# Kernel optimization log

Hardware: AMD Instinct MI355X
Metric: run time of the kernel (lower is better)

Reference implementation:

```python
import jax, jax.numpy as jnp
import numpy as np
from jax import lax

B = 8192
HS = 64        # hidden_size (output channels)
HS4 = HS + 4   # internal channel count (68)
K = 3          # conv kernel size


def setup_inputs() -> dict:
    key = jax.random.key(0)
    ks = jax.random.split(key, 16)
    def n(k, shape, s=1.0):
        return jax.random.normal(k, shape, dtype=jnp.float32) * s
    return {
        "x": n(ks[0], (B, HS, 6, 6)),
        "cell": n(ks[1], (B, 2)),
        "interspace_coord": n(ks[2], (B, 2, 6, 6)),
        "conv1_w": n(ks[3], (HS4, HS4, K, K), 0.05),
        "conv1_b": n(ks[4], (HS4,), 0.05),
        "conv3_w": n(ks[5], (HS4, HS4, K, K), 0.05),
        "conv3_b": n(ks[6], (HS4,), 0.05),
        "lin5_w": n(ks[7], (9 * HS, HS4 * 25), 0.02),
        "lin5_b": n(ks[8], (9 * HS,), 0.02),
        "lin4_w": n(ks[9], (9 * HS, HS4 * 16), 0.02),
        "lin4_b": n(ks[10], (9 * HS,), 0.02),
        "lin3_w": n(ks[11], (9 * HS, HS4 * 9), 0.02),
        "lin3_b": n(ks[12], (9 * HS,), 0.02),
        "final_w": n(ks[13], (HS, 9 * HS), 0.02),
        "final_b": n(ks[14], (HS,), 0.02),
    }


def _conv(z, w, b):
    # torch Conv2d with padding=k//2, stride 1 == SAME conv, NCHW/OIHW
    y = lax.conv_general_dilated(z, w, (1, 1), 'SAME',
                                 dimension_numbers=('NCHW', 'OIHW', 'NCHW'))
    return y + b[None, :, None, None]


def _corners(z, ws):
    # four corner windows, stacked on a new leading axis (corner-major)
    H, W = z.shape[-2:]
    return jnp.stack([z[..., :ws, :ws],
                      z[..., :ws, W - ws:],
                      z[..., H - ws:, :ws],
                      z[..., H - ws:, W - ws:]], axis=0)


def reference(x, cell, interspace_coord,
              conv1_w, conv1_b, conv3_w, conv3_b,
              lin5_w, lin5_b, lin4_w, lin4_b, lin3_w, lin3_b,
              final_w, final_b):
    Bn = x.shape[0]
    new_cell = jnp.broadcast_to(cell.reshape(Bn, -1)[:, :, None, None],
                                (Bn, 2, 6, 6))
    lins = {5: (lin5_w, lin5_b), 4: (lin4_w, lin4_b), 3: (lin3_w, lin3_b)}
    for ws in (5, 4, 3):
        z = jnp.concatenate([x, new_cell, interspace_coord], axis=1)  # [B,68,6,6]
        z = _corners(z, ws).reshape(-1, HS4, ws, ws)                  # [4B,68,ws,ws]
        z = jnp.sin(z) + jnp.cos(z)
        z = jax.nn.relu(_conv(z, conv1_w, conv1_b))
        z = jnp.sin(z) + jnp.cos(z)
        z = jax.nn.relu(_conv(z, conv3_w, conv3_b)).reshape(4, Bn, -1)
        Wl, bl = lins[ws]
        z = jax.nn.relu(z @ Wl.T + bl).reshape(4, Bn, HS, 3, 3)
        m = jnp.concatenate([z[0], z[1]], axis=-1)   # [B,64,3,6]
        n = jnp.concatenate([z[2], z[3]], axis=-1)
        x = jnp.concatenate([m, n], axis=-2)          # [B,64,6,6]
    ew = 3
    c = _corners(x, ew)                               # [4,B,64,3,3]
    c = c.reshape(4 * Bn, -1) @ final_w.T + final_b   # [4B,64]
    c = c.reshape(Bn, HS, 2, 2)                       # same flat-order reshape as torch
    xc = x[:, :, ew - 1:ew + 1, ew - 1:ew + 1]        # center 2x2
    return (xc * c).reshape(Bn, HS, -1)
```

## Files before the change

### kernel.cpp

```cpp
#include <hip/hip_runtime.h>
#include <hip/hip_bf16.h>
#include <cstdint>
#include <cstddef>

#define BN 8192
#define MTOT 32768

using bf16 = __hip_bfloat16;
typedef float f32x4 __attribute__((ext_vector_type(4)));
typedef short short8 __attribute__((ext_vector_type(8)));

__device__ __forceinline__ bf16 f2b(float v) { return __float2bfloat16(v); }
__device__ __forceinline__ float b2f(bf16 v) { return __bfloat162float(v); }
__device__ __forceinline__ float sincos_sum(float x) {
    return 1.41421356237f * __sinf(x + 0.78539816340f);
}


__global__ __launch_bounds__(256)
void zprep_block(const float* __restrict__ xF, const float* __restrict__ cell,
                 const float* __restrict__ isc, bf16* __restrict__ Z,
                 int m0g, int CM)
{
    constexpr int KD = 1728, KTRUE = 1700;
    const int b = blockIdx.x, tid = threadIdx.x;
    __shared__ float s[68][37];

    for (int i = tid; i < 64 * 36; i += 256) {
        int ic = i / 36, off = i % 36;
        s[ic][off] = sincos_sum(xF[((size_t)b * 64 + ic) * 36 + off]);
    }
    if (tid < 2) {
        float t = sincos_sum(cell[b * 2 + tid]);
        #pragma unroll
        for (int off = 0; off < 36; off++) s[64 + tid][off] = t;
    }
    if (tid >= 64 && tid < 136) {
        int j = tid - 64;
        int ic = j / 36, off = j % 36;
        s[66 + ic][off] = sincos_sum(isc[((size_t)b * 2 + ic) * 36 + off]);
    }
    __syncthreads();

    for (int i = tid; i < 4 * KD; i += 256) {
        int q = i / KD, k = i % KD;
        int gm = q * BN + b;
        if (gm < m0g || gm >= m0g + CM) continue;
        float v = 0.f;
        if (k < KTRUE) {
            int pi = k / 68, ic = k % 68;
            int r = (q >> 1) + pi / 5;
            int c = (q & 1) + pi % 5;
            v = s[ic][r * 6 + c];
        }
        Z[(size_t)(gm - m0g) * KD + k] = f2b(v);
    }
}

template<int WSv>
__device__ __forceinline__ bf16 conv_elem(const float* __restrict__ src, int n, int k)
{
    constexpr int KTRUE = 68 * WSv * WSv;
    float v = 0.f;
    if (n < KTRUE && k < KTRUE) {
        int po = n / 68, oc = n % 68, ro = po / WSv, co = po % WSv;
        int pi = k / 68, ic = k % 68, ri = pi / WSv, ci = pi % WSv;
        int kr = ri - ro + 1, kc = ci - co + 1;
        if (kr >= 0 && kr < 3 && kc >= 0 && kc < 3)
            v = src[((oc * 68 + ic) * 3 + kr) * 3 + kc];
    }
    return f2b(v);
}
template<int WSv>
__device__ __forceinline__ bf16 lin_elem(const float* __restrict__ wl, int n, int k)
{
    constexpr int KTRUE = 68 * WSv * WSv;
    float v = 0.f;
    if (n < 576 && k < KTRUE) {
        int pi = k / 68, ic = k % 68;
        v = wl[(size_t)n * KTRUE + ic * (WSv * WSv) + pi];
    }
    return f2b(v);
}

__global__ void megabuild(const float* __restrict__ c1w, const float* __restrict__ c3w,
                          const float* __restrict__ l5w, const float* __restrict__ l4w,
                          const float* __restrict__ l3w, const float* __restrict__ fw,
                          const float* __restrict__ c1b, const float* __restrict__ c3b,
                          const float* __restrict__ bl5, const float* __restrict__ bl4,
                          const float* __restrict__ bl3, const float* __restrict__ bfin,
                          const float* __restrict__ cell, const float* __restrict__ isc,
                          bf16* __restrict__ w1d5, bf16* __restrict__ w3d5,
                          bf16* __restrict__ w1d4, bf16* __restrict__ w3d4,
                          bf16* __restrict__ w1d3, bf16* __restrict__ w3d3,
                          bf16* __restrict__ wl5p, bf16* __restrict__ wl4p,
                          bf16* __restrict__ wl3p, bf16* __restrict__ wfp,
                          float* __restrict__ bias,
                          bf16* __restrict__ Z4, bf16* __restrict__ Z3)
{
    constexpr unsigned S0 = 2u*1792*1728, S1 = 2u*1152*1088, S2 = 2u*640*640;
    constexpr unsigned S3 = 640u*1728, S4 = 640u*1088, S5 = 640u*640;
    constexpr unsigned S6 = 128u*576, S7 = 9216;
    constexpr unsigned S8 = 4u*8192*16*4, S9 = 4u*8192*9*4, S10 = 32768u*28;
    constexpr unsigned O1=S0, O2=O1+S1, O3=O2+S2, O4=O3+S3, O5=O4+S4, O6=O5+S5,
                       O7=O6+S6, O8=O7+S7, O9=O8+S8, O10=O9+S9, OT=O10+S10;
    unsigned e = blockIdx.x * 256u + threadIdx.x;
    if (e >= OT) return;
    if (e < O1) {
        constexpr unsigned per = 1792u*1728;
        unsigned i = (e < per) ? e : e - per;
        bf16* dst = (e < per) ? w1d5 : w3d5;
        const float* src = (e < per) ? c1w : c3w;
        dst[i] = conv_elem<5>(src, (int)(i / 1728u), (int)(i % 1728u));
    } else if (e < O2) {
        unsigned i0 = e - O1; constexpr unsigned per = 1152u*1088;
        unsigned i = (i0 < per) ? i0 : i0 - per;
        bf16* dst = (i0 < per) ? w1d4 : w3d4;
        const float* src = (i0 < per) ? c1w : c3w;
        dst[i] = conv_elem<4>(src, (int)(i / 1088u), (int)(i % 1088u));
    } else if (e < O3) {
        unsigned i0 = e - O2; constexpr unsigned per = 640u*640;
        unsigned i = (i0 < per) ? i0 : i0 - per;
        bf16* dst = (i0 < per) ? w1d3 : w3d3;
        const float* src = (i0 < per) ? c1w : c3w;
        dst[i] = conv_elem<3>(src, (int)(i / 640u), (int)(i % 640u));
    } else if (e < O4) {
        unsigned i = e - O3;
        wl5p[i] = lin_elem<5>(l5w, (int)(i / 1728u), (int)(i % 1728u));
    } else if (e < O5) {
        unsigned i = e - O4;
        wl4p[i] = lin_elem<4>(l4w, (int)(i / 1088u), (int)(i % 1088u));
    } else if (e < O6) {
        unsigned i = e - O5;
        wl3p[i] = lin_elem<3>(l3w, (int)(i / 640u), (int)(i % 640u));
    } else if (e < O7) {
        unsigned i = e - O6, n = i / 576u, k = i % 576u;
        wfp[i] = (n < 64u) ? f2b(fw[n * 576u + k]) : f2b(0.f);
    } else if (e < O8) {
        int i = (int)(e - O7);
        float v = 0.f;
        if (i < 1792)      { int n = i;        if (n < 1700) v = c1b[n % 68]; }
        else if (i < 3584) { int n = i - 1792; if (n < 1700) v = c3b[n % 68]; }
        else if (i < 4736) { int n = i - 3584; if (n < 1088) v = c1b[n % 68]; }
        else if (i < 5888) { int n = i - 4736; if (n < 1088) v = c3b[n % 68]; }
        else if (i < 6528) { int n = i - 5888; if (n < 612)  v = c1b[n % 68]; }
        else if (i < 7168) { int n = i - 6528; if (n < 612)  v = c3b[n % 68]; }
        else if (i < 7808) { int n = i - 7168; if (n < 576)  v = bl5[n]; }
        else if (i < 8448) { int n = i - 7808; if (n < 576)  v = bl4[n]; }
        else if (i < 9088) { int n = i - 8448; if (n < 576)  v = bl3[n]; }
        else               { int n = i - 9088; if (n < 64)   v = bfin[n]; }
        bias[i] = v;
    } else if (e < O9) {
        unsigned i = e - O8;
        int j = (int)(i & 3u); i >>= 2;
        int pi = (int)(i & 15u); i >>= 4;
        int b = (int)(i & 8191u); int q = (int)(i >> 13);
        float t;
        if (j < 2) t = cell[b * 2 + j];
        else {
            int r = (q >> 1) * 2 + pi / 4, c = (q & 1) * 2 + pi % 4;
            t = isc[((size_t)b * 2 + (j - 2)) * 36 + r * 6 + c];
        }
        Z4[((size_t)q * BN + b) * 1088 + pi * 68 + 64 + j] = f2b(sincos_sum(t));
    } else if (e < O10) {
        unsigned i = e - O9;
        int j = (int)(i & 3u); i >>= 2;
        int pi = (int)(i % 9u); i /= 9u;
        int b = (int)(i & 8191u); int q = (int)(i >> 13);
        float t;
        if (j < 2) t = cell[b * 2 + j];
        else {
            int r = (q >> 1) * 3 + pi / 3, c = (q & 1) * 3 + pi % 3;
            t = isc[((size_t)b * 2 + (j - 2)) * 36 + r * 6 + c];
        }
        Z3[((size_t)q * BN + b) * 640 + pi * 68 + 64 + j] = f2b(sincos_sum(t));
    } else {
        unsigned i = e - O10;
        int m = (int)(i / 28u), t = (int)(i % 28u);
        Z3[(size_t)m * 640 + 612 + t] = f2b(0.f);
    }
}

__device__ __forceinline__ void gload_lds16(const bf16* g, const bf16* lds_wave_base)
{
    unsigned off = (unsigned)(uintptr_t)lds_wave_base;
    off = __builtin_amdgcn_readfirstlane(off);
    __builtin_amdgcn_global_load_lds((const __attribute__((address_space(1))) unsigned int*)g,
                                     (__attribute__((address_space(3))) unsigned int*)off,
                                     16, 0, 0);
}

__device__ __forceinline__ int imin(int a, int b) { return a < b ? a : b; }
__device__ __forceinline__ int imax(int a, int b) { return a > b ? a : b; }

template<int EPI, int WS, int WN>
__global__ __launch_bounds__(512, 4)
void gemm8(const bf16* __restrict__ A, const bf16* __restrict__ Bm, int KD,
           const float* __restrict__ bias, int ntiles,
           bf16* __restrict__ C, int ldc, int nlimit,
           int m0g, bf16* __restrict__ znext)
{
    __shared__ bf16 As[3][8192];
    __shared__ bf16 Bs[3][4096];
    const int tid = threadIdx.x;
    const int wave = tid >> 6, lane = tid & 63;
    const int l15 = lane & 15, lq = lane >> 4;
    const int wr = (wave >> 1) * 64, wc = (wave & 1) * 64;

    const int id = blockIdx.x;
    const int mt8 = (int)gridDim.x / (ntiles * 8);
    const int xcd = id & 7, local = id >> 3;
    const int m_idx = xcd * mt8 + local / ntiles;
    const int n_idx = local % ntiles;
    const int n0 = n_idx * 128, m0 = m_idx * 256;

    int s0b = 0, s0e = KD, s1b = 0, s1e = 0, s2b = 0, s2e = 0;
    if (WS > 0) {
        int po_lo = imin(n0 / 68, WS * WS - 1);
        int po_hi = imin((n0 + 127) / 68, WS * WS - 1);
        int ro_lo = po_lo / WS, ro_hi = po_hi / WS;
        int r_lo = imax(ro_lo - 1, 0), r_hi = imin(ro_hi + 1, WS - 1);
        int ci_lo = 0, ci_hi = WS - 1;
        if (ro_lo == ro_hi) {
            ci_lo = imax(po_lo % WS - 1, 0);
            ci_hi = imin(po_hi % WS + 1, WS - 1);
        }
        if (ci_lo == 0 && ci_hi == WS - 1) {
            s0b = (r_lo * WS * 68) & ~31;
            s0e = imin(KD, ((r_hi + 1) * WS * 68 + 31) & ~31);
        } else {
            s0b = ((r_lo * WS + ci_lo) * 68) & ~31;
            s0e = imin(KD, (((r_lo * WS + ci_hi + 1) * 68) + 31) & ~31);
            if (r_hi > r_lo) {
                s1b = (((r_lo + 1) * WS + ci_lo) * 68) & ~31;
                s1e = imin(KD, ((((r_lo + 1) * WS + ci_hi + 1) * 68) + 31) & ~31);
            }
            if (r_hi > r_lo + 1) {
                s2b = (((r_lo + 2) * WS + ci_lo) * 68) & ~31;
                s2e = imin(KD, ((((r_lo + 2) * WS + ci_hi + 1) * 68) + 31) & ~31);
            }
        }
    }
    const int c0 = (s0e - s0b) >> 5;
    const int c1 = c0 + ((s1e - s1b) >> 5);
    const int nt = c1 + ((s2e - s2b) >> 5);
    auto k0_of = [&](int t2) -> int {
        int k = s0b + (t2 << 5);
        if (t2 >= c0) k = s1b + ((t2 - c0) << 5);
        if (t2 >= c1) k = s2b + ((t2 - c1) << 5);
        return k;
    };

    const int srow = tid >> 2;
    const int sc8 = (tid & 3) ^ ((srow >> 1) & 3);
    const bf16* aSrc = A + (size_t)(m0 + srow) * KD + sc8 * 8;
    const bf16* bSrc = Bm + (size_t)(n0 + srow) * KD + sc8 * 8;
    const int sOff = srow * 32 + (tid & 3) * 8;

    auto stageA = [&](int k0, int buf) {
        gload_lds16(aSrc + k0, &As[buf][sOff]);
        gload_lds16(aSrc + k0 + (size_t)128 * KD, &As[buf][sOff + 4096]);
    };
    auto stageB = [&](int k0, int buf) {
        gload_lds16(bSrc + k0, &Bs[buf][sOff]);
    };

    const int swz = (lq ^ ((l15 >> 1) & 3)) * 8;
    const int offA0 = (wr + l15) * 32 + swz;
    const int offB0 = (wc + l15) * 32 + swz;

    f32x4 acc[4][4];
    #pragma unroll
    for (int i = 0; i < 4; i++)
        #pragma unroll
        for (int j = 0; j < 4; j++) { f32x4 z = {0.f, 0.f, 0.f, 0.f}; acc[i][j] = z; }

    {
        const int k0a = k0_of(0);
        stageA(k0a, 0); stageB(k0a, 0);
        if (nt > 1) {
            const int k0b = k0_of(1);
            stageA(k0b, 1); stageB(k0b, 1);
        }
        __syncthreads();
    }

    for (int t = 0; t < nt; ++t) {
        const int cur = t % 3;
        const int nx = (t + 2) % 3;
        const bool pf = (t + 2) < nt;

        const bf16* Ac = &As[cur][0];
        const bf16* Bc = &Bs[cur][0];

        short8 af[4], bg[4];
        #pragma unroll
        for (int i = 0; i < 4; i++) af[i] = *(const short8*)&Ac[offA0 + i * 512];
        #pragma unroll
        for (int j = 0; j < 4; j++) bg[j] = *(const short8*)&Bc[offB0 + j * 512];

        if (pf) {
            const int k2 = k0_of(t + 2);
            stageA(k2, nx); stageB(k2, nx);
        }

        __builtin_amdgcn_s_setprio(1);
        #pragma unroll
        for (int i = 0; i < 4; i++)
            #pragma unroll
            for (int j = 0; j < 4; j++)
                acc[i][j] = __builtin_amdgcn_mfma_f32_16x16x32_bf16(af[i], bg[j], acc[i][j], 0, 0, 0);
        __builtin_amdgcn_s_setprio(0);

        if (pf) asm volatile("s_waitcnt vmcnt(3)" ::: "memory");
        else    asm volatile("s_waitcnt vmcnt(0)" ::: "memory");
        __builtin_amdgcn_s_barrier();
    }

    float bj[4];
    #pragma unroll
    for (int j = 0; j < 4; j++) bj[j] = bias[n0 + wc + j * 16 + l15];

    #pragma unroll
    for (int i = 0; i < 4; i++) {
        #pragma unroll
        for (int j = 0; j < 4; j++) {
            int n = n0 + wc + j * 16 + l15;
            #pragma unroll
            for (int r = 0; r < 4; r++) {
                int m = m0 + wr + i * 16 + lq * 4 + r;
                float v = acc[i][j][r];
                if (EPI == 0) {
                    if (n < nlimit) {
                        v += bj[j]; v = fmaxf(v, 0.f); v = sincos_sum(v);
                        C[(size_t)m * ldc + n] = f2b(v);
                    }
                } else if (EPI == 1) {
                    if (n < nlimit) {
                        v += bj[j]; v = fmaxf(v, 0.f);
                        C[(size_t)m * ldc + n] = f2b(v);
                    }
                } else {
                    if (n < 576) {
                        v += bj[j]; v = fmaxf(v, 0.f);
                        bf16 tv = f2b(sincos_sum(v));
                        int gm = m0g + m;
                        int q = gm >> 13, b = gm & (BN - 1);
                        int ch = n / 9, p = n % 9;
                        int R = p / 3 + (q >> 1) * 3, Cc = p % 3 + (q & 1) * 3;
                        constexpr int OFF = 6 - WN;
                        constexpr int KDN = (WN == 4) ? 1088 : 640;
                        #pragma unroll
                        for (int qr = 0; qr < 2; qr++) {
                            int rr = R - OFF * qr;
                            if (rr < 0 || rr >= WN) continue;
                            #pragma unroll
                            for (int qc = 0; qc < 2; qc++) {
                                int cc = Cc - OFF * qc;
                                if (cc < 0 || cc >= WN) continue;
                                int pi = rr * WN + cc;
                                znext[((size_t)((qr * 2 + qc) * BN + b)) * KDN + pi * 68 + ch] = tv;
                            }
                        }
                    }
                }
            }
        }
    }
}

template<int EPI, int WS, int WN>
__global__ __launch_bounds__(256)
void gemm_bt(const bf16* __restrict__ A, const bf16* __restrict__ Bm, int KD,
             const float* __restrict__ bias, int ntiles,
             bf16* __restrict__ C, int ldc, int nlimit,
             int m0g, bf16* __restrict__ znext,
             const bf16* __restrict__ afin_xc, float* __restrict__ outp)
{
    __shared__ bf16 As[128 * 32];
    __shared__ bf16 Bs[128 * 32];
    const int tid = threadIdx.x;
    const int wave = tid >> 6, lane = tid & 63;
    const int l15 = lane & 15, lq = lane >> 4;
    const int wr = (wave >> 1) * 64, wc = (wave & 1) * 64;

    const int id = blockIdx.x;
    const int mt8 = (int)gridDim.x / (ntiles * 8);
    const int xcd = id & 7, local = id >> 3;
    const int m_idx = xcd * mt8 + local / ntiles;
    const int n_idx = local % ntiles;
    const int n0 = n_idx * 128, m0 = m_idx * 128;

    int nspans = 1, sbeg[4], send[4];
    sbeg[0] = 0; send[0] = KD;
    if (WS > 0) {
        int po_lo = imin(n0 / 68, WS * WS - 1);
        int po_hi = imin((n0 + 127) / 68, WS * WS - 1);
        int ro_lo = po_lo / WS, ro_hi = po_hi / WS;
        int r_lo = imax(ro_lo - 1, 0), r_hi = imin(ro_hi + 1, WS - 1);
        int ci_lo = 0, ci_hi = WS - 1;
        if (ro_lo == ro_hi) {
            ci_lo = imax(po_lo % WS - 1, 0);
            ci_hi = imin(po_hi % WS + 1, WS - 1);
        }
        if (ci_lo == 0 && ci_hi == WS - 1) {
            sbeg[0] = (r_lo * WS * 68) & ~31;
            send[0] = imin(KD, ((r_hi + 1) * WS * 68 + 31) & ~31);
        } else {
            nspans = 0;
            for (int ri = r_lo; ri <= r_hi; ri++) {
                sbeg[nspans] = ((ri * WS + ci_lo) * 68) & ~31;
                send[nspans] = imin(KD, (((ri * WS + ci_hi + 1) * 68) + 31) & ~31);
                nspans++;
            }
        }
    }

    float bj[4];
    #pragma unroll
    for (int j = 0; j < 4; j++) bj[j] = bias[n0 + wc + j * 16 + l15];

    const bf16* Ab = A + (size_t)m0 * KD;
    const bf16* Bb = Bm + (size_t)n0 * KD;
    const int srow = tid >> 2, scol = (tid & 3) * 8;
    const bf16* aG0 = Ab + (size_t)srow * KD + scol;
    const bf16* aG1 = Ab + (size_t)(srow + 64) * KD + scol;
    const bf16* bG0 = Bb + (size_t)srow * KD + scol;
    const bf16* bG1 = Bb + (size_t)(srow + 64) * KD + scol;
    const bf16* lA0 = &As[wave * 512];
    const bf16* lA1 = &As[2048 + wave * 512];
    const bf16* lB0 = &Bs[wave * 512];
    const bf16* lB1 = &Bs[2048 + wave * 512];

    f32x4 acc[4][4];
    #pragma unroll
    for (int i = 0; i < 4; i++)
        #pragma unroll
        for (int j = 0; j < 4; j++) { f32x4 z = {0.f, 0.f, 0.f, 0.f}; acc[i][j] = z; }

    for (int s = 0; s < nspans; s++) {
        for (int k0 = sbeg[s]; k0 < send[s]; k0 += 32) {
            gload_lds16(aG0 + k0, lA0);
            gload_lds16(aG1 + k0, lA1);
            gload_lds16(bG0 + k0, lB0);
            gload_lds16(bG1 + k0, lB1);
            __syncthreads();
            short8 af[4], bg[4];
            #pragma unroll
            for (int i = 0; i < 4; i++) af[i] = *(const short8*)&As[(wr + i * 16 + l15) * 32 + lq * 8];
            #pragma unroll
            for (int j = 0; j < 4; j++) bg[j] = *(const short8*)&Bs[(wc + j * 16 + l15) * 32 + lq * 8];
            #pragma unroll
            for (int i = 0; i < 4; i++)
                #pragma unroll
                for (int j = 0; j < 4; j++)
                    acc[i][j] = __builtin_amdgcn_mfma_f32_16x16x32_bf16(af[i], bg[j], acc[i][j], 0, 0, 0);
            __syncthreads();
        }
    }

    #pragma unroll
    for (int i = 0; i < 4; i++) {
        #pragma unroll
        for (int j = 0; j < 4; j++) {
            int n = n0 + wc + j * 16 + l15;
            #pragma unroll
            for (int r = 0; r < 4; r++) {
                int m = m0 + wr + i * 16 + lq * 4 + r;
                float v = acc[i][j][r];
                if (EPI == 0) {
                    if (n < nlimit) {
                        v += bj[j]; v = fmaxf(v, 0.f); v = sincos_sum(v);
                        C[(size_t)m * ldc + n] = f2b(v);
                    }
                } else if (EPI == 1) {
                    if (n < nlimit) {
                        v += bj[j]; v = fmaxf(v, 0.f);
                        C[(size_t)m * ldc + n] = f2b(v);
                    }
                } else if (EPI == 2) {
                    if (n < 576) {
                        v += bj[j]; v = fmaxf(v, 0.f);
                        bf16 t = f2b(sincos_sum(v));
                        int gm = m0g + m;
                        int q = gm >> 13, b = gm & (BN - 1);
                        int ch = n / 9, p = n % 9;
                        int R = p / 3 + (q >> 1) * 3, Cc = p % 3 + (q & 1) * 3;
                        constexpr int OFF = 6 - WN;
                        constexpr int KDN = (WN == 4) ? 1088 : 640;
                        #pragma unroll
                        for (int qr = 0; qr < 2; qr++) {
                            int rr = R - OFF * qr;
                            if (rr < 0 || rr >= WN) continue;
                            #pragma unroll
                            for (int qc = 0; qc < 2; qc++) {
                                int cc = Cc - OFF * qc;
                                if (cc < 0 || cc >= WN) continue;
                                int pi = rr * WN + cc;
                                znext[((size_t)((qr * 2 + qc) * BN + b)) * KDN + pi * 68 + ch] = t;
                            }
                        }
                    }
                } else {
                    if (n < 64) {
                        v += bj[j];
                        int gm = m0g + m;
                        int f = gm * 64 + n;
                        int b2 = f >> 8, rem = f & 255;
                        int ch2 = rem >> 2, ii = (rem >> 1) & 1, jj = rem & 1;
                        int qq = ii * 2 + jj;
                        const int offt[4] = {8, 6, 2, 0};
                        float xc = b2f(afin_xc[((size_t)qq * BN + b2) * 576 + ch2 * 9 + offt[qq]]);
                        outp[f] = v * xc;
                    }
                }
            }
        }
    }
}

extern "C" void kernel_launch(void* const* d_in, const int* in_sizes, int n_in,
                              void* d_out, int out_size, void* d_ws, size_t ws_size,
                              hipStream_t stream)
{
    const float* x    = (const float*)d_in[0];
    const float* cell = (const float*)d_in[1];
    const float* isc  = (const float*)d_in[2];
    const float* c1w  = (const float*)d_in[3];
    const float* c1b  = (const float*)d_in[4];
    const float* c3w  = (const float*)d_in[5];
    const float* c3b  = (const float*)d_in[6];
    const float* l5w  = (const float*)d_in[7];
    const float* l5b  = (const float*)d_in[8];
    const float* l4w  = (const float*)d_in[9];
    const float* l4b  = (const float*)d_in[10];
    const float* l3w  = (const float*)d_in[11];
    const float* l3b  = (const float*)d_in[12];
    const float* fw   = (const float*)d_in[13];
    const float* fb   = (const float*)d_in[14];

    char* base = (char*)d_ws;
    size_t cur = 0;
    auto take = [&](size_t bytes) -> char* {
        char* r = base + cur; cur += (bytes + 255) & ~(size_t)255; return r;
    };

    const size_t Z4B = (size_t)MTOT * 1088 * 2;
    const size_t Z3B = (size_t)MTOT * 640 * 2;
    const size_t AFB = (size_t)MTOT * 576 * 2;
    size_t wbytes = 2 * (1792ull * 1728 + 1152ull * 1088 + 640ull * 640) * 2
                  + (640ull * 1728 + 640ull * 1088 + 640ull * 640) * 2
                  + 128ull * 576 * 2 + 9216ull * 4 + 64 * 256;
    auto need = [&](int nc) -> size_t {
        return Z4B + Z3B + AFB + wbytes + 2 * ((size_t)(MTOT / nc) * 1728 * 2);
    };
    int nchunk = (ws_size >= need(1)) ? 1 : (ws_size >= need(2)) ? 2
               : (ws_size >= need(4)) ? 4 : (ws_size >= need(8)) ? 8 : 16;

    bf16* Z4   = (bf16*)take(Z4B);
    bf16* Z3   = (bf16*)take(Z3B);
    bf16* afinb = (bf16*)take(AFB);
    bf16* w1d5 = (bf16*)take(1792ull * 1728 * 2);
    bf16* w3d5 = (bf16*)take(1792ull * 1728 * 2);
    bf16* w1d4 = (bf16*)take(1152ull * 1088 * 2);
    bf16* w3d4 = (bf16*)take(1152ull * 1088 * 2);
    bf16* w1d3 = (bf16*)take(640ull * 640 * 2);
    bf16* w3d3 = (bf16*)take(640ull * 640 * 2);
    bf16* wl5p = (bf16*)take(640ull * 1728 * 2);
    bf16* wl4p = (bf16*)take(640ull * 1088 * 2);
    bf16* wl3p = (bf16*)take(640ull * 640 * 2);
    bf16* wfp  = (bf16*)take(128ull * 576 * 2);
    float* biasb = (float*)take(9216ull * 4);
    int CM = MTOT / nchunk;
    int mt = CM / 128;
    int mt2 = CM / 256;
    bf16* Za = (bf16*)take((size_t)CM * 1728 * 2);
    bf16* Zb = (bf16*)take((size_t)CM * 1728 * 2);

    {
        constexpr unsigned OT = 2u*1792*1728 + 2u*1152*1088 + 2u*640*640
                              + 640u*1728 + 640u*1088 + 640u*640 + 128u*576 + 9216
                              + 4u*8192*16*4 + 4u*8192*9*4 + 32768u*28;
        megabuild<<<(OT + 255) / 256, 256, 0, stream>>>(
            c1w, c3w, l5w, l4w, l3w, fw, c1b, c3b, l5b, l4b, l3b, fb, cell, isc,
            w1d5, w3d5, w1d4, w3d4, w1d3, w3d3, wl5p, wl4p, wl3p, wfp, biasb, Z4, Z3);
    }

    for (int c = 0; c < nchunk; c++) {
        int m0g = c * CM;
        zprep_block<<<BN, 256, 0, stream>>>(x, cell, isc, Za, m0g, CM);
        gemm8<0, 5, 0><<<14 * mt2, 512, 0, stream>>>(Za, w1d5, 1728, biasb + 0, 14,
                                                     Zb, 1728, 1728, 0, nullptr);
        gemm8<1, 5, 0><<<14 * mt2, 512, 0, stream>>>(Zb, w3d5, 1728, biasb + 1792, 14,
                                                     Za, 1728, 1728, 0, nullptr);
        gemm8<2, 0, 4><<<5 * mt2, 512, 0, stream>>>(Za, wl5p, 1728, biasb + 7168, 5,
                                                    nullptr, 0, 0, m0g, Z4);
    }
    for (int c = 0; c < nchunk; c++) {
        int m0g = c * CM;
        gemm8<0, 4, 0><<<9 * mt2, 512, 0, stream>>>(Z4 + (size_t)m0g * 1088, w1d4, 1088,
                                                    biasb + 3584, 9, Zb, 1088, 1088,
                                                    0, nullptr);
        gemm8<1, 4, 0><<<9 * mt2, 512, 0, stream>>>(Zb, w3d4, 1088, biasb + 4736, 9,
                                                    Za, 1088, 1088, 0, nullptr);
        gemm8<2, 0, 3><<<5 * mt2, 512, 0, stream>>>(Za, wl4p, 1088, biasb + 7808, 5,
                                                    nullptr, 0, 0, m0g, Z3);
    }
    for (int c = 0; c < nchunk; c++) {
        int m0g = c * CM;
        gemm8<0, 3, 0><<<5 * mt2, 512, 0, stream>>>(Z3 + (size_t)m0g * 640, w1d3, 640,
                                                    biasb + 5888, 5, Zb, 640, 640,
                                                    0, nullptr);
        gemm8<1, 3, 0><<<5 * mt2, 512, 0, stream>>>(Zb, w3d3, 640, biasb + 6528, 5,
                                                    Za, 640, 640, 0, nullptr);
        gemm8<1, 0, 0><<<5 * mt2, 512, 0, stream>>>(Za, wl3p, 640, biasb + 8448, 5,
                                                    afinb + (size_t)m0g * 576, 576, 576,
                                                    0, nullptr);
    }
    for (int c = 0; c < nchunk; c++) {
        int m0g = c * CM;
        gemm_bt<3, 0, 0><<<mt, 256, 0, stream>>>(afinb + (size_t)m0g * 576, wfp, 576,
                                                 biasb + 9088, 1, nullptr, 0, 0, m0g,
                                                 nullptr, afinb, (float*)d_out);
    }
}
```

Before: 1.228 ms.

## Make gemm8 persistent with wide-tile variant and vectorize zprep stores

The GEMM kernel becomes persistent: a fixed grid of 512 blocks loops over tiles, with an XCD-aware mapping of m tiles. A WIDE template variant uses 128x256 tiles for the ws=5 convolution GEMMs, so fewer n-tiles are needed and A rows are reused across a wider N. zprep now packs eight bf16 values into one 16-byte store instead of writing scalars. The persistent loop reduces launch and tail overhead but can unbalance load when the tile count does not divide evenly, and the wide tiles change how much of the banded K range each tile skips.

```diff
diff --git a/kernel.cpp b/kernel.cpp
--- a/kernel.cpp
+++ b/kernel.cpp
@@ -42,18 +42,26 @@
     }
     __syncthreads();
 
-    for (int i = tid; i < 4 * KD; i += 256) {
-        int q = i / KD, k = i % KD;
+    for (int i = tid; i < 4 * (KD / 8); i += 256) {
+        int q = i / (KD / 8), j8 = i % (KD / 8);
         int gm = q * BN + b;
         if (gm < m0g || gm >= m0g + CM) continue;
-        float v = 0.f;
-        if (k < KTRUE) {
-            int pi = k / 68, ic = k % 68;
-            int r = (q >> 1) + pi / 5;
-            int c = (q & 1) + pi % 5;
-            v = s[ic][r * 6 + c];
-        }
-        Z[(size_t)(gm - m0g) * KD + k] = f2b(v);
+        int kbase = j8 * 8;
+        short8 pack;
+        #pragma unroll
+        for (int u = 0; u < 8; u++) {
+            int k = kbase + u;
+            float v = 0.f;
+            if (k < KTRUE) {
+                int pi = k / 68, ic = k % 68;
+                int r = (q >> 1) + pi / 5;
+                int c = (q & 1) + pi % 5;
+                v = s[ic][r * 6 + c];
+            }
+            bf16 bv = f2b(v);
+            pack[u] = *reinterpret_cast<short*>(&bv);
+        }
+        *reinterpret_cast<short8*>(&Z[(size_t)(gm - m0g) * KD + kbase]) = pack;
     }
 }
 
@@ -193,173 +201,177 @@
 __device__ __forceinline__ int imin(int a, int b) { return a < b ? a : b; }
 __device__ __forceinline__ int imax(int a, int b) { return a > b ? a : b; }
 
-template<int EPI, int WS, int WN>
+template<int EPI, int WS, int WN, int WIDE>
 __global__ __launch_bounds__(512, 4)
 void gemm8(const bf16* __restrict__ A, const bf16* __restrict__ Bm, int KD,
-           const float* __restrict__ bias, int ntiles,
+           const float* __restrict__ bias, int ntiles, int mtiles,
            bf16* __restrict__ C, int ldc, int nlimit,
            int m0g, bf16* __restrict__ znext)
 {
-    __shared__ bf16 As[3][8192];
-    __shared__ bf16 Bs[3][4096];
+    constexpr int BMc = WIDE ? 128 : 256;
+    constexpr int BNc = WIDE ? 256 : 128;
+    constexpr int NWN = WIDE ? 4 : 2;
+    __shared__ bf16 As[3][BMc * 32];
+    __shared__ bf16 Bs[3][BNc * 32];
     const int tid = threadIdx.x;
     const int wave = tid >> 6, lane = tid & 63;
     const int l15 = lane & 15, lq = lane >> 4;
-    const int wr = (wave >> 1) * 64, wc = (wave & 1) * 64;
-
-    const int id = blockIdx.x;
-    const int mt8 = (int)gridDim.x / (ntiles * 8);
-    const int xcd = id & 7, local = id >> 3;
-    const int m_idx = xcd * mt8 + local / ntiles;
-    const int n_idx = local % ntiles;
-    const int n0 = n_idx * 128, m0 = m_idx * 256;
-
-    int s0b = 0, s0e = KD, s1b = 0, s1e = 0, s2b = 0, s2e = 0;
-    if (WS > 0) {
-        int po_lo = imin(n0 / 68, WS * WS - 1);
-        int po_hi = imin((n0 + 127) / 68, WS * WS - 1);
-        int ro_lo = po_lo / WS, ro_hi = po_hi / WS;
-        int r_lo = imax(ro_lo - 1, 0), r_hi = imin(ro_hi + 1, WS - 1);
-        int ci_lo = 0, ci_hi = WS - 1;
-        if (ro_lo == ro_hi) {
-            ci_lo = imax(po_lo % WS - 1, 0);
-            ci_hi = imin(po_hi % WS + 1, WS - 1);
-        }
-        if (ci_lo == 0 && ci_hi == WS - 1) {
-            s0b = (r_lo * WS * 68) & ~31;
-            s0e = imin(KD, ((r_hi + 1) * WS * 68 + 31) & ~31);
-        } else {
-            s0b = ((r_lo * WS + ci_lo) * 68) & ~31;
-            s0e = imin(KD, (((r_lo * WS + ci_hi + 1) * 68) + 31) & ~31);
-            if (r_hi > r_lo) {
-                s1b = (((r_lo + 1) * WS + ci_lo) * 68) & ~31;
-                s1e = imin(KD, ((((r_lo + 1) * WS + ci_hi + 1) * 68) + 31) & ~31);
-            }
-            if (r_hi > r_lo + 1) {
-                s2b = (((r_lo + 2) * WS + ci_lo) * 68) & ~31;
-                s2e = imin(KD, ((((r_lo + 2) * WS + ci_hi + 1) * 68) + 31) & ~31);
-            }
-        }
-    }
-    const int c0 = (s0e - s0b) >> 5;
-    const int c1 = c0 + ((s1e - s1b) >> 5);
-    const int nt = c1 + ((s2e - s2b) >> 5);
-    auto k0_of = [&](int t2) -> int {
-        int k = s0b + (t2 << 5);
-        if (t2 >= c0) k = s1b + ((t2 - c0) << 5);
-        if (t2 >= c1) k = s2b + ((t2 - c1) << 5);
-        return k;
-    };
+    const int wr = (wave / NWN) * 64, wc = (wave % NWN) * 64;
+
+    const int xcd = blockIdx.x & 7, lblk = blockIdx.x >> 3;
+    const int bpx = (int)gridDim.x >> 3;
+    const int mloc = mtiles >> 3;
+    const int tot = mloc * ntiles;
 
     const int srow = tid >> 2;
-    const int sc8 = (tid & 3) ^ ((srow >> 1) & 3);
-    const bf16* aSrc = A + (size_t)(m0 + srow) * KD + sc8 * 8;
-    const bf16* bSrc = Bm + (size_t)(n0 + srow) * KD + sc8 * 8;
+    const int scx = (tid & 3) ^ ((srow >> 1) & 3);
     const int sOff = srow * 32 + (tid & 3) * 8;
-
-    auto stageA = [&](int k0, int buf) {
-        gload_lds16(aSrc + k0, &As[buf][sOff]);
-        gload_lds16(aSrc + k0 + (size_t)128 * KD, &As[buf][sOff + 4096]);
-    };
-    auto stageB = [&](int k0, int buf) {
-        gload_lds16(bSrc + k0, &Bs[buf][sOff]);
-    };
-
     const int swz = (lq ^ ((l15 >> 1) & 3)) * 8;
     const int offA0 = (wr + l15) * 32 + swz;
     const int offB0 = (wc + l15) * 32 + swz;
 
-    f32x4 acc[4][4];
-    #pragma unroll
-    for (int i = 0; i < 4; i++)
-        #pragma unroll
-        for (int j = 0; j < 4; j++) { f32x4 z = {0.f, 0.f, 0.f, 0.f}; acc[i][j] = z; }
-
-    {
-        const int k0a = k0_of(0);
-        stageA(k0a, 0); stageB(k0a, 0);
-        if (nt > 1) {
-            const int k0b = k0_of(1);
-            stageA(k0b, 1); stageB(k0b, 1);
-        }
-        __syncthreads();
-    }
-
-    for (int t = 0; t < nt; ++t) {
-        const int cur = t % 3;
-        const int nx = (t + 2) % 3;
-        const bool pf = (t + 2) < nt;
-
-        const bf16* Ac = &As[cur][0];
-        const bf16* Bc = &Bs[cur][0];
-
-        short8 af[4], bg[4];
-        #pragma unroll
-        for (int i = 0; i < 4; i++) af[i] = *(const short8*)&Ac[offA0 + i * 512];
-        #pragma unroll
-        for (int j = 0; j < 4; j++) bg[j] = *(const short8*)&Bc[offB0 + j * 512];
-
-        if (pf) {
-            const int k2 = k0_of(t + 2);
-            stageA(k2, nx); stageB(k2, nx);
-        }
-
-        __builtin_amdgcn_s_setprio(1);
+    for (int w = lblk; w < tot; w += bpx) {
+        const int m_idx = (w / ntiles) * 8 + xcd;
+        const int n_idx = w % ntiles;
+        const int n0 = n_idx * BNc, m0 = m_idx * BMc;
+
+        int s0b = 0, s0e = KD, s1b = 0, s1e = 0, s2b = 0, s2e = 0;
+        if (WS > 0) {
+            int po_lo = imin(n0 / 68, WS * WS - 1);
+            int po_hi = imin((n0 + BNc - 1) / 68, WS * WS - 1);
+            int ro_lo = po_lo / WS, ro_hi = po_hi / WS;
+            int r_lo = imax(ro_lo - 1, 0), r_hi = imin(ro_hi + 1, WS - 1);
+            int ci_lo = 0, ci_hi = WS - 1;
+            if (ro_lo == ro_hi) {
+                ci_lo = imax(po_lo % WS - 1, 0);
+                ci_hi = imin(po_hi % WS + 1, WS - 1);
+            }
+            if (ci_lo == 0 && ci_hi == WS - 1) {
+                s0b = (r_lo * WS * 68) & ~31;
+                s0e = imin(KD, ((r_hi + 1) * WS * 68 + 31) & ~31);
+            } else {
+                s0b = ((r_lo * WS + ci_lo) * 68) & ~31;
+                s0e = imin(KD, (((r_lo * WS + ci_hi + 1) * 68) + 31) & ~31);
+                if (r_hi > r_lo) {
+                    s1b = (((r_lo + 1) * WS + ci_lo) * 68) & ~31;
+                    s1e = imin(KD, ((((r_lo + 1) * WS + ci_hi + 1) * 68) + 31) & ~31);
+                }
+                if (r_hi > r_lo + 1) {
+                    s2b = (((r_lo + 2) * WS + ci_lo) * 68) & ~31;
+                    s2e = imin(KD, ((((r_lo + 2) * WS + ci_hi + 1) * 68) + 31) & ~31);
+                }
+            }
+        }
+        const int c0 = (s0e - s0b) >> 5;
+        const int c1 = c0 + ((s1e - s1b) >> 5);
+        const int nt = c1 + ((s2e - s2b) >> 5);
+        auto k0_of = [&](int t2) -> int {
+            int k = s0b + (t2 << 5);
+            if (t2 >= c0) k = s1b + ((t2 - c0) << 5);
+            if (t2 >= c1) k = s2b + ((t2 - c1) << 5);
+            return k;
+        };
+
+        const bf16* aSrc = A + (size_t)(m0 + srow) * KD + scx * 8;
+        const bf16* bSrc = Bm + (size_t)(n0 + srow) * KD + scx * 8;
+
+        auto stageAll = [&](int k0, int buf) {
+            if (WIDE) {
+                gload_lds16(aSrc + k0, &As[buf][sOff]);
+                gload_lds16(bSrc + k0, &Bs[buf][sOff]);
+                gload_lds16(bSrc + k0 + (size_t)128 * KD, &Bs[buf][sOff + 4096]);
+            } else {
+                gload_lds16(aSrc + k0, &As[buf][sOff]);
+                gload_lds16(aSrc + k0 + (size_t)128 * KD, &As[buf][sOff + 4096]);
+                gload_lds16(bSrc + k0, &Bs[buf][sOff]);
+            }
+        };
+
+        f32x4 acc[4][4];
         #pragma unroll
         for (int i = 0; i < 4; i++)
             #pragma unroll
-            for (int j = 0; j < 4; j++)
-                acc[i][j] = __builtin_amdgcn_mfma_f32_16x16x32_bf16(af[i], bg[j], acc[i][j], 0, 0, 0);
-        __builtin_amdgcn_s_setprio(0);
-
-        if (pf) asm volatile("s_waitcnt vmcnt(3)" ::: "memory");
-        else    asm volatile("s_waitcnt vmcnt(0)" ::: "memory");
-        __builtin_amdgcn_s_barrier();
-    }
-
-    float bj[4];
-    #pragma unroll
-    for (int j = 0; j < 4; j++) bj[j] = bias[n0 + wc + j * 16 + l15];
-
-    #pragma unroll
-    for (int i = 0; i < 4; i++) {
+            for (int j = 0; j < 4; j++) { f32x4 z = {0.f, 0.f, 0.f, 0.f}; acc[i][j] = z; }
+
+        {
+            stageAll(k0_of(0), 0);
+            if (nt > 1) stageAll(k0_of(1), 1);
+            __syncthreads();
+        }
+
+        for (int t = 0; t < nt; ++t) {
+            const int cur = t % 3;
+            const int nx = (t + 2) % 3;
+            const bool pf = (t + 2) < nt;
+
+            const bf16* Ac = &As[cur][0];
+            const bf16* Bc = &Bs[cur][0];
+
+            short8 af[4], bg[4];
+            #pragma unroll
+            for (int i = 0; i < 4; i++) af[i] = *(const short8*)&Ac[offA0 + i * 512];
+            #pragma unroll
+            for (int j = 0; j < 4; j++) bg[j] = *(const short8*)&Bc[offB0 + j * 512];
+
+            if (pf) stageAll(k0_of(t + 2), nx);
+
+            __builtin_amdgcn_s_setprio(1);
+            #pragma unroll
+            for (int i = 0; i < 4; i++)
+                #pragma unroll
+                for (int j = 0; j < 4; j++)
+                    acc[i][j] = __builtin_amdgcn_mfma_f32_16x16x32_bf16(af[i], bg[j], acc[i][j], 0, 0, 0);
+            __builtin_amdgcn_s_setprio(0);
+
+            if (pf) asm volatile("s_waitcnt vmcnt(3)" ::: "memory");
+            else    asm volatile("s_waitcnt vmcnt(0)" ::: "memory");
+            __builtin_amdgcn_s_barrier();
+        }
+
+        float bj[4];
         #pragma unroll
-        for (int j = 0; j < 4; j++) {
-            int n = n0 + wc + j * 16 + l15;
-            #pragma unroll
-            for (int r = 0; r < 4; r++) {
-                int m = m0 + wr + i * 16 + lq * 4 + r;
-                float v = acc[i][j][r];
-                if (EPI == 0) {
-                    if (n < nlimit) {
-                        v += bj[j]; v = fmaxf(v, 0.f); v = sincos_sum(v);
-                        C[(size_t)m * ldc + n] = f2b(v);
-                    }
-                } else if (EPI == 1) {
-                    if (n < nlimit) {
-                        v += bj[j]; v = fmaxf(v, 0.f);
-                        C[(size_t)m * ldc + n] = f2b(v);
-                    }
-                } else {
-                    if (n < 576) {
-                        v += bj[j]; v = fmaxf(v, 0.f);
-                        bf16 tv = f2b(sincos_sum(v));
-                        int gm = m0g + m;
-                        int q = gm >> 13, b = gm & (BN - 1);
-                        int ch = n / 9, p = n % 9;
-                        int R = p / 3 + (q >> 1) * 3, Cc = p % 3 + (q & 1) * 3;
-                        constexpr int OFF = 6 - WN;
-                        constexpr int KDN = (WN == 4) ? 1088 : 640;
-                        #pragma unroll
-                        for (int qr = 0; qr < 2; qr++) {
-                            int rr = R - OFF * qr;
-                            if (rr < 0 || rr >= WN) continue;
+        for (int j = 0; j < 4; j++) bj[j] = bias[n0 + wc + j * 16 + l15];
+
+        #pragma unroll
+        for (int i = 0; i < 4; i++) {
+            #pragma unroll
+            for (int j = 0; j < 4; j++) {
+                int n = n0 + wc + j * 16 + l15;
+                #pragma unroll
+                for (int r = 0; r < 4; r++) {
+                    int m = m0 + wr + i * 16 + lq * 4 + r;
+                    float v = acc[i][j][r];
+                    if (EPI == 0) {
+                        if (n < nlimit) {
+                            v += bj[j]; v = fmaxf(v, 0.f); v = sincos_sum(v);
+                            C[(size_t)m * ldc + n] = f2b(v);
+                        }
+                    } else if (EPI == 1) {
+                        if (n < nlimit) {
+                            v += bj[j]; v = fmaxf(v, 0.f);
+                            C[(size_t)m * ldc + n] = f2b(v);
+                        }
+                    } else {
+                        if (n < 576) {
+                            v += bj[j]; v = fmaxf(v, 0.f);
+                            bf16 tv = f2b(sincos_sum(v));
+                            int gm = m0g + m;
+                            int q = gm >> 13, b = gm & (BN - 1);
+                            int ch = n / 9, p = n % 9;
+                            int R = p / 3 + (q >> 1) * 3, Cc = p % 3 + (q & 1) * 3;
+                            constexpr int OFF = 6 - WN;
+                            constexpr int KDN = (WN == 4) ? 1088 : 640;
                             #pragma unroll
-                            for (int qc = 0; qc < 2; qc++) {
-                                int cc = Cc - OFF * qc;
-                                if (cc < 0 || cc >= WN) continue;
-                                int pi = rr * WN + cc;
-                                znext[((size_t)((qr * 2 + qc) * BN + b)) * KDN + pi * 68 + ch] = tv;
+                            for (int qr = 0; qr < 2; qr++) {
+                                int rr = R - OFF * qr;
+                                if (rr < 0 || rr >= WN) continue;
+                                #pragma unroll
+                                for (int qc = 0; qc < 2; qc++) {
+                                    int cc = Cc - OFF * qc;
+                                    if (cc < 0 || cc >= WN) continue;
+                                    int pi = rr * WN + cc;
+                                    znext[((size_t)((qr * 2 + qc) * BN + b)) * KDN + pi * 68 + ch] = tv;
+                                }
                             }
                         }
                     }
@@ -589,33 +601,33 @@
     for (int c = 0; c < nchunk; c++) {
         int m0g = c * CM;
         zprep_block<<<BN, 256, 0, stream>>>(x, cell, isc, Za, m0g, CM);
-        gemm8<0, 5, 0><<<14 * mt2, 512, 0, stream>>>(Za, w1d5, 1728, biasb + 0, 14,
-                                                     Zb, 1728, 1728, 0, nullptr);
-        gemm8<1, 5, 0><<<14 * mt2, 512, 0, stream>>>(Zb, w3d5, 1728, biasb + 1792, 14,
-                                                     Za, 1728, 1728, 0, nullptr);
-        gemm8<2, 0, 4><<<5 * mt2, 512, 0, stream>>>(Za, wl5p, 1728, biasb + 7168, 5,
-                                                    nullptr, 0, 0, m0g, Z4);
+        gemm8<0, 5, 0, 1><<<512, 512, 0, stream>>>(Za, w1d5, 1728, biasb + 0, 7, mt,
+                                                   Zb, 1728, 1728, 0, nullptr);
+        gemm8<1, 5, 0, 1><<<512, 512, 0, stream>>>(Zb, w3d5, 1728, biasb + 1792, 7, mt,
+                                                   Za, 1728, 1728, 0, nullptr);
+        gemm8<2, 0, 4, 0><<<512, 512, 0, stream>>>(Za, wl5p, 1728, biasb + 7168, 5, mt2,
+                                                   nullptr, 0, 0, m0g, Z4);
     }
     for (int c = 0; c < nchunk; c++) {
         int m0g = c * CM;
-        gemm8<0, 4, 0><<<9 * mt2, 512, 0, stream>>>(Z4 + (size_t)m0g * 1088, w1d4, 1088,
-                                                    biasb + 3584, 9, Zb, 1088, 1088,
-                                                    0, nullptr);
-        gemm8<1, 4, 0><<<9 * mt2, 512, 0, stream>>>(Zb, w3d4, 1088, biasb + 4736, 9,
-                                                    Za, 1088, 1088, 0, nullptr);
-        gemm8<2, 0, 3><<<5 * mt2, 512, 0, stream>>>(Za, wl4p, 1088, biasb + 7808, 5,
-                                                    nullptr, 0, 0, m0g, Z3);
+        gemm8<0, 4, 0, 0><<<512, 512, 0, stream>>>(Z4 + (size_t)m0g * 1088, w1d4, 1088,
+                                                   biasb + 3584, 9, mt2, Zb, 1088, 1088,
+                                                   0, nullptr);
+        gemm8<1, 4, 0, 0><<<512, 512, 0, stream>>>(Zb, w3d4, 1088, biasb + 4736, 9, mt2,
+                                                   Za, 1088, 1088, 0, nullptr);
+        gemm8<2, 0, 3, 0><<<512, 512, 0, stream>>>(Za, wl4p, 1088, biasb + 7808, 5, mt2,
+                                                   nullptr, 0, 0, m0g, Z3);
     }
     for (int c = 0; c < nchunk; c++) {
         int m0g = c * CM;
-        gemm8<0, 3, 0><<<5 * mt2, 512, 0, stream>>>(Z3 + (size_t)m0g * 640, w1d3, 640,
-                                                    biasb + 5888, 5, Zb, 640, 640,
-                                                    0, nullptr);
-        gemm8<1, 3, 0><<<5 * mt2, 512, 0, stream>>>(Zb, w3d3, 640, biasb + 6528, 5,
-                                                    Za, 640, 640, 0, nullptr);
-        gemm8<1, 0, 0><<<5 * mt2, 512, 0, stream>>>(Za, wl3p, 640, biasb + 8448, 5,
-                                                    afinb + (size_t)m0g * 576, 576, 576,
-                                                    0, nullptr);
+        gemm8<0, 3, 0, 0><<<512, 512, 0, stream>>>(Z3 + (size_t)m0g * 640, w1d3, 640,
+                                                   biasb + 5888, 5, mt2, Zb, 640, 640,
+                                                   0, nullptr);
+        gemm8<1, 3, 0, 0><<<512, 512, 0, stream>>>(Zb, w3d3, 640, biasb + 6528, 5, mt2,
+                                                   Za, 640, 640, 0, nullptr);
+        gemm8<1, 0, 0, 0><<<512, 512, 0, stream>>>(Za, wl3p, 640, biasb + 8448, 5, mt2,
+                                                   afinb + (size_t)m0g * 576, 576, 576,
+                                                   0, nullptr);
     }
     for (int c = 0; c < nchunk; c++) {
         int m0g = c * CM;
```

Result: no change. 1.243 ms (+1.2%).
